# Kernel tuning notes

Measured on AMD Instinct MI355X. Metric: run time of the kernel, lower is better.

## Reference

```python
import jax, jax.numpy as jnp
import numpy as np

EPS = 1e-5
TAU = 2.0
HEADS = 8
SCALE = 0.125


def _bn(y, g, b, m, v):
    # y: [TB, C, N]; per-channel eval-mode batchnorm
    inv = jax.lax.rsqrt(v + EPS)
    return (y - m[:, None]) * (g * inv)[:, None] + b[:, None]


def _lif(x_seq, vth):
    # spikingjelly MultiStepLIFNode: v += (x - v)/tau, spike = H(v - vth), hard reset v*(1-s)
    def step(mem, xt):
        mem = mem + (xt - mem) / TAU
        s = (mem >= vth).astype(xt.dtype)
        mem = mem * (1.0 - s)
        return mem, s
    _, spikes = jax.lax.scan(step, jnp.zeros_like(x_seq[0]), x_seq)
    return spikes


def setup_inputs() -> dict:
    key = jax.random.key(0)
    ks = jax.random.split(key, 8)
    T, B, C, H, W = 4, 16, 256, 32, 32
    d = {
        'x': jax.random.normal(ks[0], (T, B, C, H, W), jnp.float32),
        'res_attn': jnp.zeros((1,), jnp.float32),
    }
    for i, p in enumerate(['q', 'k', 'v']):
        d[p + '_w'] = jax.random.normal(ks[1 + i], (C, C), jnp.float32) * 0.02
        d[p + '_gamma'] = jnp.ones((C,), jnp.float32)
        d[p + '_beta'] = jnp.zeros((C,), jnp.float32)
        d[p + '_mean'] = jnp.zeros((C,), jnp.float32)
        d[p + '_var'] = jnp.ones((C,), jnp.float32)
    d['p_w'] = jax.random.normal(ks[4], (C, C), jnp.float32) * 0.02
    d['p_b'] = jnp.zeros((C,), jnp.float32)
    d['p_gamma'] = jnp.ones((C,), jnp.float32)
    d['p_beta'] = jnp.zeros((C,), jnp.float32)
    d['p_mean'] = jnp.zeros((C,), jnp.float32)
    d['p_var'] = jnp.ones((C,), jnp.float32)
    return d


def reference(x, res_attn, q_w, q_gamma, q_beta, q_mean, q_var,
              k_w, k_gamma, k_beta, k_mean, k_var,
              v_w, v_gamma, v_beta, v_mean, v_var,
              p_w, p_b, p_gamma, p_beta, p_mean, p_var):
    T, B, C, H, W = x.shape
    N = H * W
    d = C // HEADS
    x2 = x.reshape(T * B, C, N)

    def branch(w, g, b, m, v):
        y = _bn(jnp.einsum('oc,bcn->bon', w, x2), g, b, m, v).reshape(T, B, C, N)
        s = _lif(y, 1.0)  # [T,B,C,N]
        # -> [T,B,heads,N,d]
        return s.transpose(0, 1, 3, 2).reshape(T, B, N, HEADS, d).transpose(0, 1, 3, 2, 4)

    q = branch(q_w, q_gamma, q_beta, q_mean, q_var)
    k = branch(k_w, k_gamma, k_beta, k_mean, k_var)
    v = branch(v_w, v_gamma, v_beta, v_mean, v_var)

    kv = jnp.einsum('tbhnd,tbhne->tbhde', k, v)      # [T,B,h,d,d]
    attn = jnp.einsum('tbhnd,tbhde->tbhne', q, kv) * SCALE  # [T,B,h,N,d]
    xa = attn.transpose(0, 1, 2, 4, 3).reshape(T, B, C, N)
    xa = _lif(xa, 0.5)

    y = _bn(jnp.einsum('oc,bcn->bon', p_w, xa.reshape(T * B, C, N)) + p_b[:, None],
            p_gamma, p_beta, p_mean, p_var)
    out = _lif(y.reshape(T, B, C, H, W), 1.0)
    return (out, v)
```

## Files before the change

### kernel.cpp

```cpp
#include <hip/hip_runtime.h>
#include <stdint.h>

typedef unsigned int u32;
typedef unsigned short ushort_t;

#define T_ 4
#define B_ 16
#define C_ 256
#define N_ 1024
#define CN (C_ * N_)
#define M_ELEMS (64 * C_ * N_)

#define OFF_S    0ull
#define OFF_XC   67108864ull
#define OFF_SC   67108864ull
#define OFF_KV   134217728ull
#define OFF_BNS  136314880ull
#define OFF_WC   136331264ull
#define OFF_WPC  137510912ull

typedef __attribute__((ext_vector_type(8))) short bf16x8;
typedef __attribute__((ext_vector_type(4))) float f32x4;

__device__ __forceinline__ ushort_t f2bf(float f) {
  u32 u = __float_as_uint(f);
  u32 r = (u + 0x7FFFu + ((u >> 16) & 1u)) >> 16;
  return (ushort_t)r;
}
__device__ __forceinline__ float bf2f(ushort_t h) { return __uint_as_float((u32)h << 16); }

__device__ __forceinline__ void async_copy16(const void* g, void* l) {
  __builtin_amdgcn_global_load_lds(
      (const __attribute__((address_space(1))) u32*)g,
      (__attribute__((address_space(3))) u32*)l, 16, 0, 0);
}

__device__ __forceinline__ void mfma_grp(const ushort_t* Ap, int aoff,
                                         bf16x8 b0, bf16x8 b1, bf16x8 b2, bf16x8 b3,
                                         f32x4* acc) {
  bf16x8 a0 = *(const bf16x8*)&Ap[aoff + 0 * 16 * 32];
  bf16x8 a1 = *(const bf16x8*)&Ap[aoff + 1 * 16 * 32];
  bf16x8 a2 = *(const bf16x8*)&Ap[aoff + 2 * 16 * 32];
  bf16x8 a3 = *(const bf16x8*)&Ap[aoff + 3 * 16 * 32];
  acc[0]  = __builtin_amdgcn_mfma_f32_16x16x32_bf16(a0, b0, acc[0],  0, 0, 0);
  acc[1]  = __builtin_amdgcn_mfma_f32_16x16x32_bf16(a0, b1, acc[1],  0, 0, 0);
  acc[2]  = __builtin_amdgcn_mfma_f32_16x16x32_bf16(a0, b2, acc[2],  0, 0, 0);
  acc[3]  = __builtin_amdgcn_mfma_f32_16x16x32_bf16(a0, b3, acc[3],  0, 0, 0);
  acc[4]  = __builtin_amdgcn_mfma_f32_16x16x32_bf16(a1, b0, acc[4],  0, 0, 0);
  acc[5]  = __builtin_amdgcn_mfma_f32_16x16x32_bf16(a1, b1, acc[5],  0, 0, 0);
  acc[6]  = __builtin_amdgcn_mfma_f32_16x16x32_bf16(a1, b2, acc[6],  0, 0, 0);
  acc[7]  = __builtin_amdgcn_mfma_f32_16x16x32_bf16(a1, b3, acc[7],  0, 0, 0);
  acc[8]  = __builtin_amdgcn_mfma_f32_16x16x32_bf16(a2, b0, acc[8],  0, 0, 0);
  acc[9]  = __builtin_amdgcn_mfma_f32_16x16x32_bf16(a2, b1, acc[9],  0, 0, 0);
  acc[10] = __builtin_amdgcn_mfma_f32_16x16x32_bf16(a2, b2, acc[10], 0, 0, 0);
  acc[11] = __builtin_amdgcn_mfma_f32_16x16x32_bf16(a2, b3, acc[11], 0, 0, 0);
  acc[12] = __builtin_amdgcn_mfma_f32_16x16x32_bf16(a3, b0, acc[12], 0, 0, 0);
  acc[13] = __builtin_amdgcn_mfma_f32_16x16x32_bf16(a3, b1, acc[13], 0, 0, 0);
  acc[14] = __builtin_amdgcn_mfma_f32_16x16x32_bf16(a3, b2, acc[14], 0, 0, 0);
  acc[15] = __builtin_amdgcn_mfma_f32_16x16x32_bf16(a3, b3, acc[15], 0, 0, 0);
}

__global__ void bn_prep(const float* __restrict__ qg, const float* __restrict__ qb2, const float* __restrict__ qm, const float* __restrict__ qv,
                        const float* __restrict__ kg, const float* __restrict__ kb, const float* __restrict__ km, const float* __restrict__ kvv,
                        const float* __restrict__ vg, const float* __restrict__ vb, const float* __restrict__ vm, const float* __restrict__ vv,
                        const float* __restrict__ pbias,
                        const float* __restrict__ pg, const float* __restrict__ pbt, const float* __restrict__ pm, const float* __restrict__ pv,
                        float* __restrict__ bns) {
  int i = threadIdx.x;
  int br = i >> 8, c = i & 255;
  const float *g, *bt, *m, *v;
  float bias = 0.f;
  if (br == 0)      { g = qg; bt = qb2; m = qm; v = qv; }
  else if (br == 1) { g = kg; bt = kb;  m = km; v = kvv; }
  else if (br == 2) { g = vg; bt = vb;  m = vm; v = vv; }
  else              { g = pg; bt = pbt; m = pm; v = pv; bias = pbias[c]; }
  float sc = g[c] / sqrtf(v[c] + 1e-5f);
  float sh = bt[c] + (bias - m[c]) * sc;
  float rcp = (sc != 0.f) ? (1.f / sc) : 0.f;
  *(float4*)&bns[4 * i] = make_float4(sc, sh, rcp, 0.f);
}

__global__ __launch_bounds__(256) void convert_w(const float* __restrict__ qw, const float* __restrict__ kw,
                                                 const float* __restrict__ vw, const float* __restrict__ pw,
                                                 ushort_t* __restrict__ Wc, ushort_t* __restrict__ Wpc) {
  int id = blockIdx.x * 256 + threadIdx.x;
  int br = id >> 16, o = (id >> 8) & 255, c = id & 255;
  const float* w = (br == 0) ? qw : (br == 1) ? kw : (br == 2) ? vw : pw;
  float f = w[o * 256 + c];
  ushort_t hi = f2bf(f);
  ushort_t lo = f2bf(f - bf2f(hi));
  if (br < 3) {
    ushort_t* d = Wc + (size_t)br * 196608 + (size_t)o * 768 + c;
    d[0] = hi; d[256] = lo; d[512] = hi;
  } else {
    ushort_t* d = Wpc + (size_t)o * 512 + c;
    d[0] = hi; d[256] = lo;
  }
}

__global__ __launch_bounds__(256) void convert_x(const float* __restrict__ x, ushort_t* __restrict__ Xc) {
  __shared__ ushort_t hi[32][260];
  __shared__ ushort_t lo[32][260];
  int bid = blockIdx.x;
  int nc = bid & 3, kb = (bid >> 2) & 7, tb = bid >> 5;
  int t = threadIdx.x;
  int n0 = nc * 256;
  const float* xb = x + (size_t)tb * CN + (size_t)(kb * 32) * N_ + n0;
#pragma unroll
  for (int p = 0; p < 8; ++p) {
    int k = p * 4 + (t >> 6);
    int n4 = (t & 63) * 4;
    float4 v = *(const float4*)&xb[(size_t)k * N_ + n4];
    ushort_t h0 = f2bf(v.x), h1 = f2bf(v.y), h2 = f2bf(v.z), h3 = f2bf(v.w);
    short4 hv = make_short4((short)h0, (short)h1, (short)h2, (short)h3);
    short4 lv = make_short4((short)f2bf(v.x - bf2f(h0)), (short)f2bf(v.y - bf2f(h1)),
                            (short)f2bf(v.z - bf2f(h2)), (short)f2bf(v.w - bf2f(h3)));
    *(short4*)&hi[k][n4] = hv;
    *(short4*)&lo[k][n4] = lv;
  }
  __syncthreads();
  ushort_t* Hs = Xc + ((size_t)(tb * 16 + kb) * 1024 + n0) * 32;
  ushort_t* Ls = Xc + ((size_t)(tb * 16 + 8 + kb) * 1024 + n0) * 32;
  int kq = t & 3;
#pragma unroll
  for (int q = 0; q < 4; ++q) {
    int n = q * 64 + (t >> 2);
    u32 a0 = (u32)hi[kq * 8 + 0][n] | ((u32)hi[kq * 8 + 1][n] << 16);
    u32 a1 = (u32)hi[kq * 8 + 2][n] | ((u32)hi[kq * 8 + 3][n] << 16);
    u32 a2 = (u32)hi[kq * 8 + 4][n] | ((u32)hi[kq * 8 + 5][n] << 16);
    u32 a3 = (u32)hi[kq * 8 + 6][n] | ((u32)hi[kq * 8 + 7][n] << 16);
    *(uint4*)(Hs + (size_t)n * 32 + kq * 8) = make_uint4(a0, a1, a2, a3);
    u32 b0 = (u32)lo[kq * 8 + 0][n] | ((u32)lo[kq * 8 + 1][n] << 16);
    u32 b1 = (u32)lo[kq * 8 + 2][n] | ((u32)lo[kq * 8 + 3][n] << 16);
    u32 b2 = (u32)lo[kq * 8 + 4][n] | ((u32)lo[kq * 8 + 5][n] << 16);
    u32 b3 = (u32)lo[kq * 8 + 6][n] | ((u32)lo[kq * 8 + 7][n] << 16);
    *(uint4*)(Ls + (size_t)n * 32 + kq * 8) = make_uint4(b0, b1, b2, b3);
  }
}

__global__ __launch_bounds__(256, 3) void gemm_qkv_lif(
    const ushort_t* __restrict__ Wc, const ushort_t* __restrict__ Xc,
    const float* __restrict__ bns, uint8_t* __restrict__ S) {
  __shared__ ushort_t Ah[2][4096];
  __shared__ ushort_t Xl[2][4096];
  __shared__ ushort_t Bh[2][4096];
  const int nt = blockIdx.x, mt = blockIdx.y, b = blockIdx.z;
  const int br = mt >> 1, rh = mt & 1;
  const ushort_t* Ab = Wc + (size_t)br * 196608 + (size_t)(rh * 128) * 768;
  const int tid = threadIdx.x;
  const int lane = tid & 63;
  const int quad = lane >> 4, r = lane & 15;
  const int w = tid >> 6;
  const int moff = (w & 1) * 64, noff = (w >> 1) * 64;
  const int c0 = tid, c1 = tid + 256;
  const int aoff = (moff + r) * 32 + quad * 8;
  const int boff = (noff + r) * 32 + quad * 8;

  f32x4 acc[16];
#pragma unroll
  for (int f = 0; f < 16; ++f) acc[f] = (f32x4){0.f, 0.f, 0.f, 0.f};

  for (int t = 0; t < 4; ++t) {
    const ushort_t* Xtb = Xc + (size_t)(t * 16 + b) * 16 * 32768 + (size_t)(nt * 128) * 32;
    for (int p = 0; p < 4; ++p) {
      const ushort_t* AcH = Ab + p * 64;
      const ushort_t* AcL = Ab + 256 + p * 64;
      const ushort_t* Bh0 = Xtb + (size_t)(2 * p) * 32768;
      const ushort_t* Bh1 = Bh0 + 32768;
      async_copy16(AcH + (size_t)(c0 >> 2) * 768 + (c0 & 3) * 8,      &Ah[0][c0 * 8]);
      async_copy16(AcH + (size_t)(c1 >> 2) * 768 + (c1 & 3) * 8,      &Ah[0][c1 * 8]);
      async_copy16(AcH + (size_t)(c0 >> 2) * 768 + 32 + (c0 & 3) * 8, &Ah[1][c0 * 8]);
      async_copy16(AcH + (size_t)(c1 >> 2) * 768 + 32 + (c1 & 3) * 8, &Ah[1][c1 * 8]);
      async_copy16(AcL + (size_t)(c0 >> 2) * 768 + (c0 & 3) * 8,      &Xl[0][c0 * 8]);
      async_copy16(AcL + (size_t)(c1 >> 2) * 768 + (c1 & 3) * 8,      &Xl[0][c1 * 8]);
      async_copy16(AcL + (size_t)(c0 >> 2) * 768 + 32 + (c0 & 3) * 8, &Xl[1][c0 * 8]);
      async_copy16(AcL + (size_t)(c1 >> 2) * 768 + 32 + (c1 & 3) * 8, &Xl[1][c1 * 8]);
      async_copy16(Bh0 + c0 * 8, &Bh[0][c0 * 8]);
      async_copy16(Bh0 + c1 * 8, &Bh[0][c1 * 8]);
      async_copy16(Bh1 + c0 * 8, &Bh[1][c0 * 8]);
      async_copy16(Bh1 + c1 * 8, &Bh[1][c1 * 8]);
      __syncthreads();
      {
        bf16x8 b0 = *(const bf16x8*)&Bh[0][boff + 0 * 16 * 32];
        bf16x8 b1 = *(const bf16x8*)&Bh[0][boff + 1 * 16 * 32];
        bf16x8 b2 = *(const bf16x8*)&Bh[0][boff + 2 * 16 * 32];
        bf16x8 b3 = *(const bf16x8*)&Bh[0][boff + 3 * 16 * 32];
        mfma_grp(&Ah[0][0], aoff, b0, b1, b2, b3, acc);
        mfma_grp(&Xl[0][0], aoff, b0, b1, b2, b3, acc);
      }
      {
        bf16x8 b0 = *(const bf16x8*)&Bh[1][boff + 0 * 16 * 32];
        bf16x8 b1 = *(const bf16x8*)&Bh[1][boff + 1 * 16 * 32];
        bf16x8 b2 = *(const bf16x8*)&Bh[1][boff + 2 * 16 * 32];
        bf16x8 b3 = *(const bf16x8*)&Bh[1][boff + 3 * 16 * 32];
        mfma_grp(&Ah[1][0], aoff, b0, b1, b2, b3, acc);
        mfma_grp(&Xl[1][0], aoff, b0, b1, b2, b3, acc);
      }
      __syncthreads();
      const ushort_t* Bl0 = Xtb + (size_t)(8 + 2 * p) * 32768;
      const ushort_t* Bl1 = Bl0 + 32768;
      async_copy16(Bl0 + c0 * 8, &Xl[0][c0 * 8]);
      async_copy16(Bl0 + c1 * 8, &Xl[0][c1 * 8]);
      async_copy16(Bl1 + c0 * 8, &Xl[1][c0 * 8]);
      async_copy16(Bl1 + c1 * 8, &Xl[1][c1 * 8]);
      __syncthreads();
      {
        bf16x8 b0 = *(const bf16x8*)&Xl[0][boff + 0 * 16 * 32];
        bf16x8 b1 = *(const bf16x8*)&Xl[0][boff + 1 * 16 * 32];
        bf16x8 b2 = *(const bf16x8*)&Xl[0][boff + 2 * 16 * 32];
        bf16x8 b3 = *(const bf16x8*)&Xl[0][boff + 3 * 16 * 32];
        mfma_grp(&Ah[0][0], aoff, b0, b1, b2, b3, acc);
      }
      {
        bf16x8 b0 = *(const bf16x8*)&Xl[1][boff + 0 * 16 * 32];
        bf16x8 b1 = *(const bf16x8*)&Xl[1][boff + 1 * 16 * 32];
        bf16x8 b2 = *(const bf16x8*)&Xl[1][boff + 2 * 16 * 32];
        bf16x8 b3 = *(const bf16x8*)&Xl[1][boff + 3 * 16 * 32];
        mfma_grp(&Ah[1][0], aoff, b0, b1, b2, b3, acc);
      }
      __syncthreads();
    }
    uint8_t* Sb = S + (size_t)br * M_ELEMS + (size_t)(t * 16 + b) * CN;
#pragma unroll
    for (int i = 0; i < 4; ++i) {
#pragma unroll
      for (int rg = 0; rg < 4; ++rg) {
        int c = rh * 128 + moff + i * 16 + quad * 4 + rg;
        float4 bn = *(const float4*)&bns[4 * (br * 256 + c)];
        float hsc = 0.5f * bn.x;
        float hsh = 0.5f * bn.y;
        float rcp = bn.z;
        uint8_t* row = Sb + (size_t)c * N_ + nt * 128 + noff + r;
#pragma unroll
        for (int j = 0; j < 4; ++j) {
          float m = acc[i * 4 + j][rg] * hsc + hsh;
          uint8_t s = (m >= 1.0f) ? 1 : 0;
          row[j * 16] = s;
          acc[i * 4 + j][rg] = s ? 0.f : m * rcp;
        }
      }
    }
  }
}

__global__ __launch_bounds__(256) void transpose_v(const uint8_t* __restrict__ SV, float* __restrict__ vout) {
  size_t o4 = ((size_t)blockIdx.x * 256 + threadIdx.x) * 4;
  int dd = (int)(o4 & 31);
  int n = (int)((o4 >> 5) & 1023);
  int h = (int)((o4 >> 15) & 7);
  int tb = (int)(o4 >> 18);
  const uint8_t* src = SV + (size_t)tb * CN + (size_t)(h * 32 + dd) * N_ + n;
  *(float4*)(vout + o4) = make_float4((float)src[0], (float)src[(size_t)N_],
                                      (float)src[2 * (size_t)N_], (float)src[3 * (size_t)N_]);
}

__global__ __launch_bounds__(256) void kv_gram(const uint8_t* __restrict__ SK,
                                               const uint8_t* __restrict__ SV,
                                               float* __restrict__ KV) {
  __shared__ unsigned long long Kb[32][17];
  __shared__ unsigned long long Vb[32][17];
  const int tb = blockIdx.x >> 3, h = blockIdx.x & 7;
  const uint8_t* K = SK + (size_t)tb * CN + (size_t)h * 32 * N_;
  const uint8_t* V = SV + (size_t)tb * CN + (size_t)h * 32 * N_;
  const int tid = threadIdx.x;
  const int row = tid >> 3, c8 = tid & 7;
  uint8_t* Kb8 = (uint8_t*)&Kb[row][0];
  uint8_t* Vb8 = (uint8_t*)&Vb[row][0];
#pragma unroll
  for (int i = 0; i < 16; ++i) {
    int c = c8 + 8 * i;
    unsigned long long xk = *(const unsigned long long*)(K + (size_t)row * N_ + (size_t)c * 8);
    unsigned long long xv = *(const unsigned long long*)(V + (size_t)row * N_ + (size_t)c * 8);
    Kb8[c] = (uint8_t)((xk * 0x8040201008040201ull) >> 56);
    Vb8[c] = (uint8_t)((xv * 0x8040201008040201ull) >> 56);
  }
  __syncthreads();
  const int dd = tid >> 3, e0 = (tid & 7) * 4;
  int a0 = 0, a1 = 0, a2 = 0, a3 = 0;
#pragma unroll
  for (int c = 0; c < 16; ++c) {
    unsigned long long kd = Kb[dd][c];
    a0 += __popcll(kd & Vb[e0 + 0][c]);
    a1 += __popcll(kd & Vb[e0 + 1][c]);
    a2 += __popcll(kd & Vb[e0 + 2][c]);
    a3 += __popcll(kd & Vb[e0 + 3][c]);
  }
  float* o = KV + (size_t)(tb * 8 + h) * 1024 + dd * 32 + e0;
  o[0] = (float)a0; o[1] = (float)a1; o[2] = (float)a2; o[3] = (float)a3;
}

__global__ __launch_bounds__(256) void attn_lif(const uint8_t* __restrict__ SQ,
                                                const float* __restrict__ KV,
                                                ushort_t* __restrict__ Sc) {
  __shared__ float kvs[1024];
  const int bid = blockIdx.x;
  const int nb = bid & 15, h = (bid >> 4) & 7, b = bid >> 7;
  const int n0 = nb * 64;
  const int tid = threadIdx.x;
  const int nl = tid & 63, eg = tid >> 6;
  float mem[8];
#pragma unroll
  for (int j = 0; j < 8; ++j) mem[j] = 0.f;
  for (int t = 0; t < 4; ++t) {
    const float* kvp = KV + (size_t)((t * B_ + b) * 8 + h) * 1024;
    *(float4*)&kvs[tid * 4] = *(const float4*)&kvp[tid * 4];
    __syncthreads();
    const uint8_t* q = SQ + (size_t)(t * B_ + b) * CN + (size_t)h * 32 * N_ + n0 + nl;
    float val[8];
#pragma unroll
    for (int j = 0; j < 8; ++j) val[j] = 0.f;
#pragma unroll 4
    for (int dd = 0; dd < 32; ++dd) {
      float qv = (float)q[(size_t)dd * N_];
#pragma unroll
      for (int j = 0; j < 8; ++j) val[j] += qv * kvs[dd * 32 + eg * 8 + j];
    }
    ushort_t pk[8];
#pragma unroll
    for (int j = 0; j < 8; ++j) {
      float a = val[j] * 0.125f;
      mem[j] += (a - mem[j]) * 0.5f;
      int s = (mem[j] >= 0.5f);
      pk[j] = s ? (ushort_t)0x3F80 : (ushort_t)0;
      if (s) mem[j] = 0.f;
    }
    uint4 o;
    o.x = (u32)pk[0] | ((u32)pk[1] << 16);
    o.y = (u32)pk[2] | ((u32)pk[3] << 16);
    o.z = (u32)pk[4] | ((u32)pk[5] << 16);
    o.w = (u32)pk[6] | ((u32)pk[7] << 16);
    *(uint4*)(Sc + ((size_t)((t * B_ + b) * 8 + h) * 1024 + n0 + nl) * 32 + eg * 8) = o;
    __syncthreads();
  }
}

__global__ __launch_bounds__(256, 3) void gemm_p_lif(
    const ushort_t* __restrict__ Wpc, const ushort_t* __restrict__ Sc,
    const float* __restrict__ bns, float* __restrict__ out) {
  __shared__ ushort_t Ah[2][4096];
  __shared__ ushort_t Al[2][4096];
  __shared__ ushort_t Bs[2][4096];
  const int nt = blockIdx.x, mt = blockIdx.y, b = blockIdx.z;
  const ushort_t* Ab = Wpc + (size_t)(mt * 128) * 512;
  const int tid = threadIdx.x;
  const int lane = tid & 63;
  const int quad = lane >> 4, r = lane & 15;
  const int w = tid >> 6;
  const int moff = (w & 1) * 64, noff = (w >> 1) * 64;
  const int c0 = tid, c1 = tid + 256;
  const int aoff = (moff + r) * 32 + quad * 8;
  const int boff = (noff + r) * 32 + quad * 8;
  f32x4 acc[16];
#pragma unroll
  for (int f = 0; f < 16; ++f) acc[f] = (f32x4){0.f, 0.f, 0.f, 0.f};

  for (int t = 0; t < 4; ++t) {
    const ushort_t* Stb = Sc + (size_t)(t * 16 + b) * 8 * 32768 + (size_t)(nt * 128) * 32;
    for (int p = 0; p < 4; ++p) {
      const ushort_t* AcH = Ab + p * 64;
      const ushort_t* AcL = Ab + 256 + p * 64;
      const ushort_t* Bb0 = Stb + (size_t)(2 * p) * 32768;
      const ushort_t* Bb1 = Bb0 + 32768;
      async_copy16(AcH + (size_t)(c0 >> 2) * 512 + (c0 & 3) * 8,      &Ah[0][c0 * 8]);
      async_copy16(AcH + (size_t)(c1 >> 2) * 512 + (c1 & 3) * 8,      &Ah[0][c1 * 8]);
      async_copy16(AcH + (size_t)(c0 >> 2) * 512 + 32 + (c0 & 3) * 8, &Ah[1][c0 * 8]);
      async_copy16(AcH + (size_t)(c1 >> 2) * 512 + 32 + (c1 & 3) * 8, &Ah[1][c1 * 8]);
      async_copy16(AcL + (size_t)(c0 >> 2) * 512 + (c0 & 3) * 8,      &Al[0][c0 * 8]);
      async_copy16(AcL + (size_t)(c1 >> 2) * 512 + (c1 & 3) * 8,      &Al[0][c1 * 8]);
      async_copy16(AcL + (size_t)(c0 >> 2) * 512 + 32 + (c0 & 3) * 8, &Al[1][c0 * 8]);
      async_copy16(AcL + (size_t)(c1 >> 2) * 512 + 32 + (c1 & 3) * 8, &Al[1][c1 * 8]);
      async_copy16(Bb0 + c0 * 8, &Bs[0][c0 * 8]);
      async_copy16(Bb0 + c1 * 8, &Bs[0][c1 * 8]);
      async_copy16(Bb1 + c0 * 8, &Bs[1][c0 * 8]);
      async_copy16(Bb1 + c1 * 8, &Bs[1][c1 * 8]);
      __syncthreads();
      {
        bf16x8 b0 = *(const bf16x8*)&Bs[0][boff + 0 * 16 * 32];
        bf16x8 b1 = *(const bf16x8*)&Bs[0][boff + 1 * 16 * 32];
        bf16x8 b2 = *(const bf16x8*)&Bs[0][boff + 2 * 16 * 32];
        bf16x8 b3 = *(const bf16x8*)&Bs[0][boff + 3 * 16 * 32];
        mfma_grp(&Ah[0][0], aoff, b0, b1, b2, b3, acc);
        mfma_grp(&Al[0][0], aoff, b0, b1, b2, b3, acc);
      }
      {
        bf16x8 b0 = *(const bf16x8*)&Bs[1][boff + 0 * 16 * 32];
        bf16x8 b1 = *(const bf16x8*)&Bs[1][boff + 1 * 16 * 32];
        bf16x8 b2 = *(const bf16x8*)&Bs[1][boff + 2 * 16 * 32];
        bf16x8 b3 = *(const bf16x8*)&Bs[1][boff + 3 * 16 * 32];
        mfma_grp(&Ah[1][0], aoff, b0, b1, b2, b3, acc);
        mfma_grp(&Al[1][0], aoff, b0, b1, b2, b3, acc);
      }
      __syncthreads();
    }
    float* Ob = out + (size_t)(t * 16 + b) * CN;
#pragma unroll
    for (int i = 0; i < 4; ++i) {
#pragma unroll
      for (int rg = 0; rg < 4; ++rg) {
        int c = mt * 128 + moff + i * 16 + quad * 4 + rg;
        float4 bn = *(const float4*)&bns[4 * (768 + c)];
        float hsc = 0.5f * bn.x;
        float hsh = 0.5f * bn.y;
        float rcp = bn.z;
        float* row = Ob + (size_t)c * N_ + nt * 128 + noff + r;
#pragma unroll
        for (int j = 0; j < 4; ++j) {
          float m = acc[i * 4 + j][rg] * hsc + hsh;
          int s = (m >= 1.0f);
          row[j * 16] = s ? 1.0f : 0.0f;
          acc[i * 4 + j][rg] = s ? 0.f : m * rcp;
        }
      }
    }
  }
}

extern "C" void kernel_launch(void* const* d_in, const int* in_sizes, int n_in,
                              void* d_out, int out_size, void* d_ws, size_t ws_size,
                              hipStream_t stream) {
  const float* x   = (const float*)d_in[0];
  const float* qw  = (const float*)d_in[2];
  const float* qg  = (const float*)d_in[3];
  const float* qb  = (const float*)d_in[4];
  const float* qm  = (const float*)d_in[5];
  const float* qv  = (const float*)d_in[6];
  const float* kw  = (const float*)d_in[7];
  const float* kg  = (const float*)d_in[8];
  const float* kb  = (const float*)d_in[9];
  const float* km  = (const float*)d_in[10];
  const float* kvv = (const float*)d_in[11];
  const float* vw  = (const float*)d_in[12];
  const float* vg  = (const float*)d_in[13];
  const float* vb  = (const float*)d_in[14];
  const float* vm  = (const float*)d_in[15];
  const float* vv  = (const float*)d_in[16];
  const float* pw  = (const float*)d_in[17];
  const float* pb  = (const float*)d_in[18];
  const float* pg  = (const float*)d_in[19];
  const float* pbt = (const float*)d_in[20];
  const float* pm  = (const float*)d_in[21];
  const float* pv  = (const float*)d_in[22];

  float* out = (float*)d_out;
  float* vout = out + M_ELEMS;

  uint8_t* ws = (uint8_t*)d_ws;
  uint8_t* S   = ws + OFF_S;
  ushort_t* Xc = (ushort_t*)(ws + OFF_XC);
  ushort_t* Sc = (ushort_t*)(ws + OFF_SC);
  float* KV    = (float*)(ws + OFF_KV);
  float* BNS   = (float*)(ws + OFF_BNS);
  ushort_t* Wc  = (ushort_t*)(ws + OFF_WC);
  ushort_t* Wpc = (ushort_t*)(ws + OFF_WPC);

  bn_prep<<<dim3(1), dim3(1024), 0, stream>>>(qg, qb, qm, qv, kg, kb, km, kvv,
                                              vg, vb, vm, vv, pb, pg, pbt, pm, pv, BNS);
  convert_w<<<dim3(1024), dim3(256), 0, stream>>>(qw, kw, vw, pw, Wc, Wpc);
  convert_x<<<dim3(2048), dim3(256), 0, stream>>>(x, Xc);
  gemm_qkv_lif<<<dim3(8, 6, 16), dim3(256), 0, stream>>>(Wc, Xc, BNS, S);
  transpose_v<<<dim3(16384), dim3(256), 0, stream>>>(S + 2ull * M_ELEMS, vout);
  kv_gram<<<dim3(512), dim3(256), 0, stream>>>(S + 1ull * M_ELEMS, S + 2ull * M_ELEMS, KV);
  attn_lif<<<dim3(2048), dim3(256), 0, stream>>>(S, KV, Sc);
  gemm_p_lif<<<dim3(8, 2, 16), dim3(256), 0, stream>>>(Wpc, Sc, BNS, out);
}
```

Before: 403.1 us.

## Fuse prep kernels, write v output from QKV GEMM, fuse KV gram into attention

```diff
diff --git a/kernel.cpp b/kernel.cpp
--- a/kernel.cpp
+++ b/kernel.cpp
@@ -60,87 +60,87 @@
   acc[15] = __builtin_amdgcn_mfma_f32_16x16x32_bf16(a3, b3, acc[15], 0, 0, 0);
 }
 
-__global__ void bn_prep(const float* __restrict__ qg, const float* __restrict__ qb2, const float* __restrict__ qm, const float* __restrict__ qv,
-                        const float* __restrict__ kg, const float* __restrict__ kb, const float* __restrict__ km, const float* __restrict__ kvv,
-                        const float* __restrict__ vg, const float* __restrict__ vb, const float* __restrict__ vm, const float* __restrict__ vv,
-                        const float* __restrict__ pbias,
-                        const float* __restrict__ pg, const float* __restrict__ pbt, const float* __restrict__ pm, const float* __restrict__ pv,
-                        float* __restrict__ bns) {
-  int i = threadIdx.x;
-  int br = i >> 8, c = i & 255;
-  const float *g, *bt, *m, *v;
-  float bias = 0.f;
-  if (br == 0)      { g = qg; bt = qb2; m = qm; v = qv; }
-  else if (br == 1) { g = kg; bt = kb;  m = km; v = kvv; }
-  else if (br == 2) { g = vg; bt = vb;  m = vm; v = vv; }
-  else              { g = pg; bt = pbt; m = pm; v = pv; bias = pbias[c]; }
-  float sc = g[c] / sqrtf(v[c] + 1e-5f);
-  float sh = bt[c] + (bias - m[c]) * sc;
-  float rcp = (sc != 0.f) ? (1.f / sc) : 0.f;
-  *(float4*)&bns[4 * i] = make_float4(sc, sh, rcp, 0.f);
-}
-
-__global__ __launch_bounds__(256) void convert_w(const float* __restrict__ qw, const float* __restrict__ kw,
-                                                 const float* __restrict__ vw, const float* __restrict__ pw,
-                                                 ushort_t* __restrict__ Wc, ushort_t* __restrict__ Wpc) {
-  int id = blockIdx.x * 256 + threadIdx.x;
-  int br = id >> 16, o = (id >> 8) & 255, c = id & 255;
-  const float* w = (br == 0) ? qw : (br == 1) ? kw : (br == 2) ? vw : pw;
-  float f = w[o * 256 + c];
-  ushort_t hi = f2bf(f);
-  ushort_t lo = f2bf(f - bf2f(hi));
-  if (br < 3) {
-    ushort_t* d = Wc + (size_t)br * 196608 + (size_t)o * 768 + c;
-    d[0] = hi; d[256] = lo; d[512] = hi;
-  } else {
-    ushort_t* d = Wpc + (size_t)o * 512 + c;
-    d[0] = hi; d[256] = lo;
-  }
-}
-
-__global__ __launch_bounds__(256) void convert_x(const float* __restrict__ x, ushort_t* __restrict__ Xc) {
+__global__ __launch_bounds__(256) void prep(
+    const float* __restrict__ x,
+    const float* __restrict__ qw, const float* __restrict__ kw,
+    const float* __restrict__ vw, const float* __restrict__ pw,
+    const float* __restrict__ qg, const float* __restrict__ qb2, const float* __restrict__ qm, const float* __restrict__ qv,
+    const float* __restrict__ kg, const float* __restrict__ kb, const float* __restrict__ km, const float* __restrict__ kvv,
+    const float* __restrict__ vg, const float* __restrict__ vb, const float* __restrict__ vm, const float* __restrict__ vv,
+    const float* __restrict__ pbias, const float* __restrict__ pg, const float* __restrict__ pbt,
+    const float* __restrict__ pm, const float* __restrict__ pv,
+    ushort_t* __restrict__ Xc, ushort_t* __restrict__ Wc, ushort_t* __restrict__ Wpc,
+    float* __restrict__ bns) {
   __shared__ ushort_t hi[32][260];
   __shared__ ushort_t lo[32][260];
-  int bid = blockIdx.x;
-  int nc = bid & 3, kb = (bid >> 2) & 7, tb = bid >> 5;
-  int t = threadIdx.x;
-  int n0 = nc * 256;
-  const float* xb = x + (size_t)tb * CN + (size_t)(kb * 32) * N_ + n0;
-#pragma unroll
-  for (int p = 0; p < 8; ++p) {
-    int k = p * 4 + (t >> 6);
-    int n4 = (t & 63) * 4;
-    float4 v = *(const float4*)&xb[(size_t)k * N_ + n4];
-    ushort_t h0 = f2bf(v.x), h1 = f2bf(v.y), h2 = f2bf(v.z), h3 = f2bf(v.w);
-    short4 hv = make_short4((short)h0, (short)h1, (short)h2, (short)h3);
-    short4 lv = make_short4((short)f2bf(v.x - bf2f(h0)), (short)f2bf(v.y - bf2f(h1)),
-                            (short)f2bf(v.z - bf2f(h2)), (short)f2bf(v.w - bf2f(h3)));
-    *(short4*)&hi[k][n4] = hv;
-    *(short4*)&lo[k][n4] = lv;
-  }
-  __syncthreads();
-  ushort_t* Hs = Xc + ((size_t)(tb * 16 + kb) * 1024 + n0) * 32;
-  ushort_t* Ls = Xc + ((size_t)(tb * 16 + 8 + kb) * 1024 + n0) * 32;
-  int kq = t & 3;
-#pragma unroll
-  for (int q = 0; q < 4; ++q) {
-    int n = q * 64 + (t >> 2);
-    u32 a0 = (u32)hi[kq * 8 + 0][n] | ((u32)hi[kq * 8 + 1][n] << 16);
-    u32 a1 = (u32)hi[kq * 8 + 2][n] | ((u32)hi[kq * 8 + 3][n] << 16);
-    u32 a2 = (u32)hi[kq * 8 + 4][n] | ((u32)hi[kq * 8 + 5][n] << 16);
-    u32 a3 = (u32)hi[kq * 8 + 6][n] | ((u32)hi[kq * 8 + 7][n] << 16);
-    *(uint4*)(Hs + (size_t)n * 32 + kq * 8) = make_uint4(a0, a1, a2, a3);
-    u32 b0 = (u32)lo[kq * 8 + 0][n] | ((u32)lo[kq * 8 + 1][n] << 16);
-    u32 b1 = (u32)lo[kq * 8 + 2][n] | ((u32)lo[kq * 8 + 3][n] << 16);
-    u32 b2 = (u32)lo[kq * 8 + 4][n] | ((u32)lo[kq * 8 + 5][n] << 16);
-    u32 b3 = (u32)lo[kq * 8 + 6][n] | ((u32)lo[kq * 8 + 7][n] << 16);
-    *(uint4*)(Ls + (size_t)n * 32 + kq * 8) = make_uint4(b0, b1, b2, b3);
+  const int bid = blockIdx.x;
+  const int t = threadIdx.x;
+  if (bid < 2048) {
+    int nc = bid & 3, kb = (bid >> 2) & 7, tb = bid >> 5;
+    int n0 = nc * 256;
+    const float* xb = x + (size_t)tb * CN + (size_t)(kb * 32) * N_ + n0;
+#pragma unroll
+    for (int p = 0; p < 8; ++p) {
+      int k = p * 4 + (t >> 6);
+      int n4 = (t & 63) * 4;
+      float4 v = *(const float4*)&xb[(size_t)k * N_ + n4];
+      ushort_t h0 = f2bf(v.x), h1 = f2bf(v.y), h2 = f2bf(v.z), h3 = f2bf(v.w);
+      short4 hv = make_short4((short)h0, (short)h1, (short)h2, (short)h3);
+      short4 lv = make_short4((short)f2bf(v.x - bf2f(h0)), (short)f2bf(v.y - bf2f(h1)),
+                              (short)f2bf(v.z - bf2f(h2)), (short)f2bf(v.w - bf2f(h3)));
+      *(short4*)&hi[k][n4] = hv;
+      *(short4*)&lo[k][n4] = lv;
+    }
+    __syncthreads();
+    ushort_t* Hs = Xc + ((size_t)(tb * 16 + kb) * 1024 + n0) * 32;
+    ushort_t* Ls = Xc + ((size_t)(tb * 16 + 8 + kb) * 1024 + n0) * 32;
+    int kq = t & 3;
+#pragma unroll
+    for (int q = 0; q < 4; ++q) {
+      int n = q * 64 + (t >> 2);
+      u32 a0 = (u32)hi[kq * 8 + 0][n] | ((u32)hi[kq * 8 + 1][n] << 16);
+      u32 a1 = (u32)hi[kq * 8 + 2][n] | ((u32)hi[kq * 8 + 3][n] << 16);
+      u32 a2 = (u32)hi[kq * 8 + 4][n] | ((u32)hi[kq * 8 + 5][n] << 16);
+      u32 a3 = (u32)hi[kq * 8 + 6][n] | ((u32)hi[kq * 8 + 7][n] << 16);
+      *(uint4*)(Hs + (size_t)n * 32 + kq * 8) = make_uint4(a0, a1, a2, a3);
+      u32 b0 = (u32)lo[kq * 8 + 0][n] | ((u32)lo[kq * 8 + 1][n] << 16);
+      u32 b1 = (u32)lo[kq * 8 + 2][n] | ((u32)lo[kq * 8 + 3][n] << 16);
+      u32 b2 = (u32)lo[kq * 8 + 4][n] | ((u32)lo[kq * 8 + 5][n] << 16);
+      u32 b3 = (u32)lo[kq * 8 + 6][n] | ((u32)lo[kq * 8 + 7][n] << 16);
+      *(uint4*)(Ls + (size_t)n * 32 + kq * 8) = make_uint4(b0, b1, b2, b3);
+    }
+  } else if (bid < 3072) {
+    int id = (bid - 2048) * 256 + t;
+    int br = id >> 16, o = (id >> 8) & 255, c = id & 255;
+    const float* w = (br == 0) ? qw : (br == 1) ? kw : (br == 2) ? vw : pw;
+    float f = w[o * 256 + c];
+    ushort_t hw = f2bf(f);
+    ushort_t lw = f2bf(f - bf2f(hw));
+    if (br < 3) {
+      ushort_t* d = Wc + (size_t)br * 196608 + (size_t)o * 768 + c;
+      d[0] = hw; d[256] = lw; d[512] = hw;
+    } else {
+      ushort_t* d = Wpc + (size_t)o * 512 + c;
+      d[0] = hw; d[256] = lw;
+    }
+  } else {
+    int br = bid - 3072, c = t;
+    const float *g, *bt, *m, *v;
+    float bias = 0.f;
+    if (br == 0)      { g = qg; bt = qb2; m = qm; v = qv; }
+    else if (br == 1) { g = kg; bt = kb;  m = km; v = kvv; }
+    else if (br == 2) { g = vg; bt = vb;  m = vm; v = vv; }
+    else              { g = pg; bt = pbt; m = pm; v = pv; bias = pbias[c]; }
+    float sc = g[c] / sqrtf(v[c] + 1e-5f);
+    float sh = bt[c] + (bias - m[c]) * sc;
+    float rcp = (sc != 0.f) ? (1.f / sc) : 0.f;
+    *(float4*)&bns[4 * (br * 256 + c)] = make_float4(sc, sh, rcp, 0.f);
   }
 }
 
 __global__ __launch_bounds__(256, 3) void gemm_qkv_lif(
     const ushort_t* __restrict__ Wc, const ushort_t* __restrict__ Xc,
-    const float* __restrict__ bns, uint8_t* __restrict__ S) {
+    const float* __restrict__ bns, uint8_t* __restrict__ S, float* __restrict__ vout) {
   __shared__ ushort_t Ah[2][4096];
   __shared__ ushort_t Xl[2][4096];
   __shared__ ushort_t Bh[2][4096];
@@ -231,105 +231,111 @@
         float hsh = 0.5f * bn.y;
         float rcp = bn.z;
         uint8_t* row = Sb + (size_t)c * N_ + nt * 128 + noff + r;
-#pragma unroll
-        for (int j = 0; j < 4; ++j) {
-          float m = acc[i * 4 + j][rg] * hsc + hsh;
-          uint8_t s = (m >= 1.0f) ? 1 : 0;
-          row[j * 16] = s;
-          acc[i * 4 + j][rg] = s ? 0.f : m * rcp;
+        if (br == 2) {
+          float* vr = vout + (((size_t)(t * 16 + b) * 8 + (c >> 5)) * 1024 +
+                              (size_t)(nt * 128 + noff + r)) * 32 + (c & 31);
+#pragma unroll
+          for (int j = 0; j < 4; ++j) {
+            float m = acc[i * 4 + j][rg] * hsc + hsh;
+            int s = (m >= 1.0f);
+            row[j * 16] = (uint8_t)s;
+            vr[j * 16 * 32] = s ? 1.0f : 0.0f;
+            acc[i * 4 + j][rg] = s ? 0.f : m * rcp;
+          }
+        } else {
+#pragma unroll
+          for (int j = 0; j < 4; ++j) {
+            float m = acc[i * 4 + j][rg] * hsc + hsh;
+            int s = (m >= 1.0f);
+            row[j * 16] = (uint8_t)s;
+            acc[i * 4 + j][rg] = s ? 0.f : m * rcp;
+          }
         }
       }
     }
   }
 }
 
-__global__ __launch_bounds__(256) void transpose_v(const uint8_t* __restrict__ SV, float* __restrict__ vout) {
-  size_t o4 = ((size_t)blockIdx.x * 256 + threadIdx.x) * 4;
-  int dd = (int)(o4 & 31);
-  int n = (int)((o4 >> 5) & 1023);
-  int h = (int)((o4 >> 15) & 7);
-  int tb = (int)(o4 >> 18);
-  const uint8_t* src = SV + (size_t)tb * CN + (size_t)(h * 32 + dd) * N_ + n;
-  *(float4*)(vout + o4) = make_float4((float)src[0], (float)src[(size_t)N_],
-                                      (float)src[2 * (size_t)N_], (float)src[3 * (size_t)N_]);
-}
-
-__global__ __launch_bounds__(256) void kv_gram(const uint8_t* __restrict__ SK,
-                                               const uint8_t* __restrict__ SV,
-                                               float* __restrict__ KV) {
+__global__ __launch_bounds__(256) void attn_fused(const uint8_t* __restrict__ SQ,
+                                                  const uint8_t* __restrict__ SK,
+                                                  const uint8_t* __restrict__ SV,
+                                                  ushort_t* __restrict__ Sc) {
   __shared__ unsigned long long Kb[32][17];
   __shared__ unsigned long long Vb[32][17];
-  const int tb = blockIdx.x >> 3, h = blockIdx.x & 7;
-  const uint8_t* K = SK + (size_t)tb * CN + (size_t)h * 32 * N_;
-  const uint8_t* V = SV + (size_t)tb * CN + (size_t)h * 32 * N_;
+  __shared__ float kvs[1024];
+  const int nq = blockIdx.x, h = blockIdx.y, b = blockIdx.z;
+  const int n0 = nq * 256;
   const int tid = threadIdx.x;
   const int row = tid >> 3, c8 = tid & 7;
-  uint8_t* Kb8 = (uint8_t*)&Kb[row][0];
-  uint8_t* Vb8 = (uint8_t*)&Vb[row][0];
-#pragma unroll
-  for (int i = 0; i < 16; ++i) {
-    int c = c8 + 8 * i;
-    unsigned long long xk = *(const unsigned long long*)(K + (size_t)row * N_ + (size_t)c * 8);
-    unsigned long long xv = *(const unsigned long long*)(V + (size_t)row * N_ + (size_t)c * 8);
-    Kb8[c] = (uint8_t)((xk * 0x8040201008040201ull) >> 56);
-    Vb8[c] = (uint8_t)((xv * 0x8040201008040201ull) >> 56);
-  }
-  __syncthreads();
-  const int dd = tid >> 3, e0 = (tid & 7) * 4;
-  int a0 = 0, a1 = 0, a2 = 0, a3 = 0;
-#pragma unroll
-  for (int c = 0; c < 16; ++c) {
-    unsigned long long kd = Kb[dd][c];
-    a0 += __popcll(kd & Vb[e0 + 0][c]);
-    a1 += __popcll(kd & Vb[e0 + 1][c]);
-    a2 += __popcll(kd & Vb[e0 + 2][c]);
-    a3 += __popcll(kd & Vb[e0 + 3][c]);
-  }
-  float* o = KV + (size_t)(tb * 8 + h) * 1024 + dd * 32 + e0;
-  o[0] = (float)a0; o[1] = (float)a1; o[2] = (float)a2; o[3] = (float)a3;
-}
-
-__global__ __launch_bounds__(256) void attn_lif(const uint8_t* __restrict__ SQ,
-                                                const float* __restrict__ KV,
-                                                ushort_t* __restrict__ Sc) {
-  __shared__ float kvs[1024];
-  const int bid = blockIdx.x;
-  const int nb = bid & 15, h = (bid >> 4) & 7, b = bid >> 7;
-  const int n0 = nb * 64;
-  const int tid = threadIdx.x;
-  const int nl = tid & 63, eg = tid >> 6;
-  float mem[8];
-#pragma unroll
-  for (int j = 0; j < 8; ++j) mem[j] = 0.f;
+  float mem[32];
+#pragma unroll
+  for (int e = 0; e < 32; ++e) mem[e] = 0.f;
   for (int t = 0; t < 4; ++t) {
-    const float* kvp = KV + (size_t)((t * B_ + b) * 8 + h) * 1024;
-    *(float4*)&kvs[tid * 4] = *(const float4*)&kvp[tid * 4];
+    const int tb = t * 16 + b;
+    const uint8_t* Kp = SK + (size_t)tb * CN + (size_t)(h * 32 + row) * N_;
+    const uint8_t* Vp = SV + (size_t)tb * CN + (size_t)(h * 32 + row) * N_;
+    uint8_t* Kb8 = (uint8_t*)&Kb[row][0];
+    uint8_t* Vb8 = (uint8_t*)&Vb[row][0];
+#pragma unroll
+    for (int i = 0; i < 16; ++i) {
+      int c = c8 + 8 * i;
+      unsigned long long xk = *(const unsigned long long*)(Kp + (size_t)c * 8);
+      unsigned long long xv = *(const unsigned long long*)(Vp + (size_t)c * 8);
+      Kb8[c] = (uint8_t)((xk * 0x8040201008040201ull) >> 56);
+      Vb8[c] = (uint8_t)((xv * 0x8040201008040201ull) >> 56);
+    }
     __syncthreads();
-    const uint8_t* q = SQ + (size_t)(t * B_ + b) * CN + (size_t)h * 32 * N_ + n0 + nl;
-    float val[8];
-#pragma unroll
-    for (int j = 0; j < 8; ++j) val[j] = 0.f;
+    {
+      const int dd = tid >> 3, e0 = (tid & 7) * 4;
+      int a0 = 0, a1 = 0, a2 = 0, a3 = 0;
+#pragma unroll
+      for (int c = 0; c < 16; ++c) {
+        unsigned long long kd = Kb[dd][c];
+        a0 += __popcll(kd & Vb[e0 + 0][c]);
+        a1 += __popcll(kd & Vb[e0 + 1][c]);
+        a2 += __popcll(kd & Vb[e0 + 2][c]);
+        a3 += __popcll(kd & Vb[e0 + 3][c]);
+      }
+      kvs[dd * 32 + e0 + 0] = (float)a0;
+      kvs[dd * 32 + e0 + 1] = (float)a1;
+      kvs[dd * 32 + e0 + 2] = (float)a2;
+      kvs[dd * 32 + e0 + 3] = (float)a3;
+    }
+    __syncthreads();
+    const uint8_t* q = SQ + (size_t)tb * CN + (size_t)(h * 32) * N_ + n0 + tid;
+    float val[32];
+#pragma unroll
+    for (int e = 0; e < 32; ++e) val[e] = 0.f;
 #pragma unroll 4
     for (int dd = 0; dd < 32; ++dd) {
       float qv = (float)q[(size_t)dd * N_];
-#pragma unroll
-      for (int j = 0; j < 8; ++j) val[j] += qv * kvs[dd * 32 + eg * 8 + j];
-    }
-    ushort_t pk[8];
-#pragma unroll
-    for (int j = 0; j < 8; ++j) {
-      float a = val[j] * 0.125f;
-      mem[j] += (a - mem[j]) * 0.5f;
-      int s = (mem[j] >= 0.5f);
-      pk[j] = s ? (ushort_t)0x3F80 : (ushort_t)0;
-      if (s) mem[j] = 0.f;
-    }
-    uint4 o;
-    o.x = (u32)pk[0] | ((u32)pk[1] << 16);
-    o.y = (u32)pk[2] | ((u32)pk[3] << 16);
-    o.z = (u32)pk[4] | ((u32)pk[5] << 16);
-    o.w = (u32)pk[6] | ((u32)pk[7] << 16);
-    *(uint4*)(Sc + ((size_t)((t * B_ + b) * 8 + h) * 1024 + n0 + nl) * 32 + eg * 8) = o;
+      const float4* k4 = (const float4*)&kvs[dd * 32];
+#pragma unroll
+      for (int g = 0; g < 8; ++g) {
+        float4 kk = k4[g];
+        val[g * 4 + 0] += qv * kk.x;
+        val[g * 4 + 1] += qv * kk.y;
+        val[g * 4 + 2] += qv * kk.z;
+        val[g * 4 + 3] += qv * kk.w;
+      }
+    }
+    u32 pk[16];
+#pragma unroll
+    for (int e = 0; e < 32; e += 2) {
+      float a0 = val[e] * 0.125f;
+      float a1 = val[e + 1] * 0.125f;
+      mem[e] += (a0 - mem[e]) * 0.5f;
+      mem[e + 1] += (a1 - mem[e + 1]) * 0.5f;
+      int s0 = (mem[e] >= 0.5f);
+      int s1 = (mem[e + 1] >= 0.5f);
+      if (s0) mem[e] = 0.f;
+      if (s1) mem[e + 1] = 0.f;
+      pk[e >> 1] = (s0 ? 0x3F80u : 0u) | (s1 ? 0x3F800000u : 0u);
+    }
+    ushort_t* so = Sc + ((size_t)(tb * 8 + h) * 1024 + n0 + tid) * 32;
+#pragma unroll
+    for (int u = 0; u < 4; ++u)
+      ((uint4*)so)[u] = make_uint4(pk[u * 4 + 0], pk[u * 4 + 1], pk[u * 4 + 2], pk[u * 4 + 3]);
     __syncthreads();
   }
 }
@@ -402,12 +408,12 @@
         float hsc = 0.5f * bn.x;
         float hsh = 0.5f * bn.y;
         float rcp = bn.z;
-        float* row = Ob + (size_t)c * N_ + nt * 128 + noff + r;
+        float* row2 = Ob + (size_t)c * N_ + nt * 128 + noff + r;
 #pragma unroll
         for (int j = 0; j < 4; ++j) {
           float m = acc[i * 4 + j][rg] * hsc + hsh;
           int s = (m >= 1.0f);
-          row[j * 16] = s ? 1.0f : 0.0f;
+          row2[j * 16] = s ? 1.0f : 0.0f;
           acc[i * 4 + j][rg] = s ? 0.f : m * rcp;
         }
       }
@@ -448,18 +454,15 @@
   uint8_t* S   = ws + OFF_S;
   ushort_t* Xc = (ushort_t*)(ws + OFF_XC);
   ushort_t* Sc = (ushort_t*)(ws + OFF_SC);
-  float* KV    = (float*)(ws + OFF_KV);
   float* BNS   = (float*)(ws + OFF_BNS);
   ushort_t* Wc  = (ushort_t*)(ws + OFF_WC);
   ushort_t* Wpc = (ushort_t*)(ws + OFF_WPC);
 
-  bn_prep<<<dim3(1), dim3(1024), 0, stream>>>(qg, qb, qm, qv, kg, kb, km, kvv,
-                                              vg, vb, vm, vv, pb, pg, pbt, pm, pv, BNS);
-  convert_w<<<dim3(1024), dim3(256), 0, stream>>>(qw, kw, vw, pw, Wc, Wpc);
-  convert_x<<<dim3(2048), dim3(256), 0, stream>>>(x, Xc);
-  gemm_qkv_lif<<<dim3(8, 6, 16), dim3(256), 0, stream>>>(Wc, Xc, BNS, S);
-  transpose_v<<<dim3(16384), dim3(256), 0, stream>>>(S + 2ull * M_ELEMS, vout);
-  kv_gram<<<dim3(512), dim3(256), 0, stream>>>(S + 1ull * M_ELEMS, S + 2ull * M_ELEMS, KV);
-  attn_lif<<<dim3(2048), dim3(256), 0, stream>>>(S, KV, Sc);
+  prep<<<dim3(3076), dim3(256), 0, stream>>>(x, qw, kw, vw, pw,
+                                             qg, qb, qm, qv, kg, kb, km, kvv,
+                                             vg, vb, vm, vv, pb, pg, pbt, pm, pv,
+                                             Xc, Wc, Wpc, BNS);
+  gemm_qkv_lif<<<dim3(8, 6, 16), dim3(256), 0, stream>>>(Wc, Xc, BNS, S, vout);
+  attn_fused<<<dim3(4, 8, 16), dim3(256), 0, stream>>>(S, S + 1ull * M_ELEMS, S + 2ull * M_ELEMS, Sc);
   gemm_p_lif<<<dim3(8, 2, 16), dim3(256), 0, stream>>>(Wpc, Sc, BNS, out);
 }
```

After: 481.1 us. 19.4% more time.
